# Kernel tuning notes

Measured on AMD Instinct MI355X. Metric: run time of the kernel, lower is better.

## Reference

```python
import jax, jax.numpy as jnp
import numpy as np

B, C, T = 128, 295, 2048
D1 = 270
NUM_SUBJECTS = 64

def setup_inputs() -> dict:
    key = jax.random.key(0)
    k_x, k_s, k_w1, k_b1, k_ws = jax.random.split(key, 5)
    X = jax.random.normal(k_x, (B, C, T), dtype=jnp.float32)
    subject_idxs = jax.random.randint(k_s, (B,), 0, NUM_SUBJECTS)
    W1 = jax.random.normal(k_w1, (D1, C), dtype=jnp.float32) * 0.05
    b1 = jax.random.normal(k_b1, (D1,), dtype=jnp.float32) * 0.05
    Ws = jax.random.normal(k_ws, (NUM_SUBJECTS, D1, D1), dtype=jnp.float32) * 0.05
    return {"X": X, "subject_idxs": subject_idxs, "W1": W1, "b1": b1, "Ws": Ws}

def reference(X, subject_idxs, W1, b1, Ws):
    # Shared 1x1 conv: pointwise channel mix C -> D1 with bias.  [B, D1, T]
    y = jnp.einsum('dc,bct->bdt', W1, X) + b1[None, :, None]
    # Top-1 expert dispatch: gather each sample's subject matrix. [B, D1, D1]
    W_sel = Ws[subject_idxs]
    # Per-sample 1x1 conv (batched GEMM), no bias.            [B, D1, T]
    out = jnp.einsum('bed,bdt->bet', W_sel, y)
    return out
```

## Files before the change

kernel.cpp:

```cpp
#include <hip/hip_runtime.h>
#include <hip/hip_bf16.h>

#define NSUBJ 64
#define CIN   295
#define DD    270
#define TT    2048
#define BB    128

#define WF_PER_S  92160
#define WF_PER_KS 9216
#define W1T_PER_KS 10240

typedef __attribute__((ext_vector_type(8))) short bf16x8;
typedef __attribute__((ext_vector_type(4))) float f32x4;
typedef unsigned short u16;

__device__ __forceinline__ u16 f2bf(float f) {
    return __bfloat16_as_ushort(__float2bfloat16(f));
}

__device__ __forceinline__ void glds16(const void* g, void* lds_base) {
    __builtin_amdgcn_global_load_lds(
        (const __attribute__((address_space(1))) unsigned int*)g,
        (__attribute__((address_space(3))) unsigned int*)lds_base, 16, 0, 0);
}

__global__ __launch_bounds__(256) void k_prep_w1(const float* __restrict__ W1,
                                                 const float* __restrict__ b1,
                                                 u16* __restrict__ W1t)
{
    const int idx = blockIdx.x * 256 + threadIdx.x;
    const int ks = idx / W1T_PER_KS;
    const int r  = idx - ks * W1T_PER_KS;
    const int kq = r / 2560;
    const int c  = (r - kq * 2560) >> 3;
    const int k8 = r & 7;
    const int d  = ks * 32 + kq * 8 + k8;
    float v = 0.f;
    if (d < DD) {
        if (c < CIN) v = W1[d * CIN + c];
        else if (c == CIN) v = b1[d];
    }
    W1t[idx] = f2bf(v);
}

__global__ __launch_bounds__(256, 1) void k_fuse_w(const float* __restrict__ Ws,
                                                   const u16* __restrict__ W1t,
                                                   u16* __restrict__ Wf)
{
    __shared__ u16 Aw[3072];
    __shared__ u16 Bw[10240];
    const int tid = threadIdx.x, lane = tid & 63, wid = tid >> 6;
    const int wm = wid >> 1, wn = wid & 1;
    const int mt = blockIdx.x, s = blockIdx.y;
    const int e0 = mt * 96;
    const float* Wsb = Ws + (size_t)s * DD * DD;

    f32x4 acc[3][10];
#pragma unroll
    for (int i = 0; i < 3; ++i)
#pragma unroll
        for (int j = 0; j < 10; ++j) acc[i][j] = (f32x4){0.f, 0.f, 0.f, 0.f};

    for (int ks = 0; ks < 9; ++ks) {
        const int k0 = ks * 32;
#pragma unroll
        for (int ci = 0; ci < 3; ++ci) {
            const int id = tid + ci * 256;
            const int m = id >> 3, q = id & 7;
            const int e = e0 + m, d = k0 + q * 4;
            float2 v01 = {0.f, 0.f}, v23 = {0.f, 0.f};
            if (e < DD) {
                if (d < DD)     v01 = *(const float2*)(Wsb + (size_t)e * DD + d);
                if (d + 2 < DD) v23 = *(const float2*)(Wsb + (size_t)e * DD + d + 2);
            }
            ushort4 h;
            h.x = f2bf(v01.x); h.y = f2bf(v01.y); h.z = f2bf(v23.x); h.w = f2bf(v23.y);
            *(ushort4*)(&Aw[(q >> 1) * 768 + m * 8 + (q & 1) * 4]) = h;
        }
#pragma unroll
        for (int k5 = 0; k5 < 5; ++k5) {
            const int seg = wid * 5 + k5;
            glds16(W1t + (size_t)ks * W1T_PER_KS + seg * 512 + lane * 8, &Bw[seg * 512]);
        }
        __syncthreads();
        bf16x8 af[3];
#pragma unroll
        for (int i = 0; i < 3; ++i)
            af[i] = *(const bf16x8*)(&Aw[(lane >> 4) * 768 + (wm * 48 + i * 16 + (lane & 15)) * 8]);
#pragma unroll
        for (int j = 0; j < 10; ++j) {
            const bf16x8 bfj = *(const bf16x8*)(&Bw[(lane >> 4) * 2560 + (wn * 160 + j * 16 + (lane & 15)) * 8]);
#pragma unroll
            for (int i = 0; i < 3; ++i)
                acc[i][j] = __builtin_amdgcn_mfma_f32_16x16x32_bf16(af[i], bfj, acc[i][j], 0, 0, 0);
        }
        __syncthreads();
    }
    const int rb = (lane >> 4) * 4, cc = lane & 15;
#pragma unroll
    for (int i = 0; i < 3; ++i) {
#pragma unroll
        for (int r = 0; r < 4; ++r) {
            const int e = e0 + wm * 48 + i * 16 + rb + r;
#pragma unroll
            for (int j = 0; j < 10; ++j) {
                const int c = wn * 160 + j * 16 + cc;
                Wf[(size_t)s * WF_PER_S + (c >> 5) * WF_PER_KS + ((c >> 3) & 3) * 2304
                   + e * 8 + (c & 7)] = f2bf(acc[i][j][r]);
            }
        }
    }
}

__global__ __launch_bounds__(256, 2) void k_main(const float* __restrict__ X,
                                                 const int* __restrict__ subj,
                                                 const u16* __restrict__ Wf,
                                                 float* __restrict__ out)
{
    __shared__ u16   Am[2][9216];
    __shared__ float Xm[2][2048];
    const int tid = threadIdx.x, lane = tid & 63, wid = tid >> 6;
    const int wm = wid >> 1, wn = wid & 1;
    const int nt = blockIdx.x, b = blockIdx.y;
    const int t0 = nt * 64;
    const int s = subj[b];
    const float* Xb = X + (size_t)b * CIN * TT;
    const u16* WfA = Wf + (size_t)s * WF_PER_S;
    const int g = lane >> 4;

    f32x4 acc[9][2];
#pragma unroll
    for (int i = 0; i < 9; ++i)
#pragma unroll
        for (int j = 0; j < 2; ++j) acc[i][j] = (f32x4){0.f, 0.f, 0.f, 0.f};

#define STAGEA(KS)                                                          \
    {                                                                       \
        _Pragma("unroll")                                                   \
        for (int k5 = 0; k5 < 5; ++k5) {                                    \
            const int seg = wid + 4 * k5;                                   \
            if (seg < 18)                                                   \
                glds16(WfA + (size_t)(KS) * WF_PER_KS + seg * 512 + lane * 8,\
                       &Am[(KS) & 1][seg * 512]);                           \
        }                                                                   \
    }
#define STAGEX(KS)                                                          \
    {                                                                       \
        _Pragma("unroll")                                                   \
        for (int k2 = 0; k2 < 2; ++k2) {                                    \
            const int seg = wid * 2 + k2;                                   \
            const int cr0 = (KS) * 32 + seg * 4 + g;                        \
            const int cr  = (cr0 < CIN) ? cr0 : (CIN - 1);                  \
            const int sc  = (lane & 15) ^ (((seg >> 1) & 3) << 2);          \
            glds16(Xb + (size_t)cr * TT + t0 + sc * 4,                      \
                   &Xm[(KS) & 1][seg * 256]);                               \
        }                                                                   \
    }
#define COMPUTE(KS, LAST)                                                   \
    {                                                                       \
        const float* Xc = &Xm[(KS) & 1][0];                                 \
        bf16x8 bfr[2];                                                      \
        _Pragma("unroll")                                                   \
        for (int j = 0; j < 2; ++j) {                                       \
            const int tsw = (wn * 32 + j * 16 + (lane & 15)) ^ (g << 4);    \
            bf16x8 bb;                                                      \
            _Pragma("unroll")                                               \
            for (int q = 0; q < 8; ++q) {                                   \
                float v = Xc[(g * 8 + q) * 64 + tsw];                       \
                if (LAST) {                                                 \
                    if (q == 7)      v = (g == 0) ? 1.0f : 0.0f;            \
                    else if (g > 0)  v = 0.0f;                              \
                }                                                           \
                bb[q] = (short)f2bf(v);                                     \
            }                                                               \
            bfr[j] = bb;                                                    \
        }                                                                   \
        _Pragma("unroll")                                                   \
        for (int i = 0; i < 9; ++i) {                                       \
            const bf16x8 af = *(const bf16x8*)(&Am[(KS) & 1][g * 2304 + (wm * 144 + i * 16 + (lane & 15)) * 8]); \
            acc[i][0] = __builtin_amdgcn_mfma_f32_16x16x32_bf16(af, bfr[0], acc[i][0], 0, 0, 0); \
            acc[i][1] = __builtin_amdgcn_mfma_f32_16x16x32_bf16(af, bfr[1], acc[i][1], 0, 0, 0); \
        }                                                                   \
    }

    STAGEA(0); STAGEX(0);
    __syncthreads();

#pragma unroll
    for (int ks = 0; ks < 10; ++ks) {
        if (ks < 9) { STAGEA(ks + 1); STAGEX(ks + 1); }
        COMPUTE(ks, (ks == 9));
        __syncthreads();
    }

    const int rb = g * 4, cc = lane & 15;
#pragma unroll
    for (int i = 0; i < 9; ++i) {
#pragma unroll
        for (int r = 0; r < 4; ++r) {
            const int e = wm * 144 + i * 16 + rb + r;
            if (e < DD) {
#pragma unroll
                for (int j = 0; j < 2; ++j) {
                    const int t = t0 + wn * 32 + j * 16 + cc;
                    out[((size_t)b * DD + e) * TT + t] = acc[i][j][r];
                }
            }
        }
    }
#undef STAGEA
#undef STAGEX
#undef COMPUTE
}

extern "C" void kernel_launch(void* const* d_in, const int* in_sizes, int n_in,
                              void* d_out, int out_size, void* d_ws, size_t ws_size,
                              hipStream_t stream) {
    const float* X    = (const float*)d_in[0];
    const int*   subj = (const int*)d_in[1];
    const float* W1   = (const float*)d_in[2];
    const float* b1   = (const float*)d_in[3];
    const float* Ws   = (const float*)d_in[4];
    float* out = (float*)d_out;

    u16* Wf  = (u16*)d_ws;
    u16* W1t = (u16*)((char*)d_ws + (size_t)NSUBJ * WF_PER_S * 2);

    k_prep_w1<<<dim3(360), 256, 0, stream>>>(W1, b1, W1t);
    k_fuse_w<<<dim3(3, NSUBJ), 256, 0, stream>>>(Ws, W1t, Wf);
    k_main<<<dim3(TT / 64, BB), 256, 0, stream>>>(X, subj, Wf, out);
}
```

Measured before the change: 192.5 us.

## Drop LDS staging in main GEMM; load operands directly to registers, remap blocks by XCD

```diff
diff --git a/kernel.cpp b/kernel.cpp
--- a/kernel.cpp
+++ b/kernel.cpp
@@ -118,16 +118,17 @@
                                                  const u16* __restrict__ Wf,
                                                  float* __restrict__ out)
 {
-    __shared__ u16   Am[2][9216];
-    __shared__ float Xm[2][2048];
     const int tid = threadIdx.x, lane = tid & 63, wid = tid >> 6;
     const int wm = wid >> 1, wn = wid & 1;
-    const int nt = blockIdx.x, b = blockIdx.y;
+    const int g = lane >> 4, l15 = lane & 15;
+    const int hw = blockIdx.x;
+    const int w  = (hw & 7) * 512 + (hw >> 3);
+    const int b  = w >> 5, nt = w & 31;
     const int t0 = nt * 64;
-    const int s = subj[b];
+    const int s  = subj[b];
     const float* Xb = X + (size_t)b * CIN * TT;
-    const u16* WfA = Wf + (size_t)s * WF_PER_S;
-    const int g = lane >> 4;
+    const u16* aB = Wf + (size_t)s * WF_PER_S + g * 2304 + (wm * 144 + l15) * 8;
+    const int tj0 = t0 + wn * 32 + l15;
 
     f32x4 acc[9][2];
 #pragma unroll
@@ -135,66 +136,62 @@
 #pragma unroll
         for (int j = 0; j < 2; ++j) acc[i][j] = (f32x4){0.f, 0.f, 0.f, 0.f};
 
-#define STAGEA(KS)                                                          \
-    {                                                                       \
-        _Pragma("unroll")                                                   \
-        for (int k5 = 0; k5 < 5; ++k5) {                                    \
-            const int seg = wid + 4 * k5;                                   \
-            if (seg < 18)                                                   \
-                glds16(WfA + (size_t)(KS) * WF_PER_KS + seg * 512 + lane * 8,\
-                       &Am[(KS) & 1][seg * 512]);                           \
-        }                                                                   \
-    }
-#define STAGEX(KS)                                                          \
-    {                                                                       \
-        _Pragma("unroll")                                                   \
-        for (int k2 = 0; k2 < 2; ++k2) {                                    \
-            const int seg = wid * 2 + k2;                                   \
-            const int cr0 = (KS) * 32 + seg * 4 + g;                        \
-            const int cr  = (cr0 < CIN) ? cr0 : (CIN - 1);                  \
-            const int sc  = (lane & 15) ^ (((seg >> 1) & 3) << 2);          \
-            glds16(Xb + (size_t)cr * TT + t0 + sc * 4,                      \
-                   &Xm[(KS) & 1][seg * 256]);                               \
-        }                                                                   \
-    }
-#define COMPUTE(KS, LAST)                                                   \
-    {                                                                       \
-        const float* Xc = &Xm[(KS) & 1][0];                                 \
-        bf16x8 bfr[2];                                                      \
-        _Pragma("unroll")                                                   \
-        for (int j = 0; j < 2; ++j) {                                       \
-            const int tsw = (wn * 32 + j * 16 + (lane & 15)) ^ (g << 4);    \
-            bf16x8 bb;                                                      \
-            _Pragma("unroll")                                               \
-            for (int q = 0; q < 8; ++q) {                                   \
-                float v = Xc[(g * 8 + q) * 64 + tsw];                       \
-                if (LAST) {                                                 \
-                    if (q == 7)      v = (g == 0) ? 1.0f : 0.0f;            \
-                    else if (g > 0)  v = 0.0f;                              \
-                }                                                           \
-                bb[q] = (short)f2bf(v);                                     \
-            }                                                               \
-            bfr[j] = bb;                                                    \
-        }                                                                   \
-        _Pragma("unroll")                                                   \
-        for (int i = 0; i < 9; ++i) {                                       \
-            const bf16x8 af = *(const bf16x8*)(&Am[(KS) & 1][g * 2304 + (wm * 144 + i * 16 + (lane & 15)) * 8]); \
-            acc[i][0] = __builtin_amdgcn_mfma_f32_16x16x32_bf16(af, bfr[0], acc[i][0], 0, 0, 0); \
-            acc[i][1] = __builtin_amdgcn_mfma_f32_16x16x32_bf16(af, bfr[1], acc[i][1], 0, 0, 0); \
-        }                                                                   \
-    }
-
-    STAGEA(0); STAGEX(0);
-    __syncthreads();
-
-#pragma unroll
-    for (int ks = 0; ks < 10; ++ks) {
-        if (ks < 9) { STAGEA(ks + 1); STAGEX(ks + 1); }
-        COMPUTE(ks, (ks == 9));
-        __syncthreads();
-    }
-
-    const int rb = g * 4, cc = lane & 15;
+#pragma unroll
+    for (int ks = 0; ks < 9; ++ks) {
+        bf16x8 af[9];
+#pragma unroll
+        for (int i = 0; i < 9; ++i)
+            af[i] = *(const bf16x8*)(aB + (size_t)ks * WF_PER_KS + i * 128);
+        float x0[8], x1[8];
+#pragma unroll
+        for (int q = 0; q < 8; ++q) {
+            const size_t roff = (size_t)((ks * 32 + g * 8 + q)) * TT + tj0;
+            x0[q] = Xb[roff];
+            x1[q] = Xb[roff + 16];
+        }
+        bf16x8 b0, b1;
+#pragma unroll
+        for (int q = 0; q < 8; ++q) {
+            b0[q] = (short)f2bf(x0[q]);
+            b1[q] = (short)f2bf(x1[q]);
+        }
+#pragma unroll
+        for (int i = 0; i < 9; ++i) {
+            acc[i][0] = __builtin_amdgcn_mfma_f32_16x16x32_bf16(af[i], b0, acc[i][0], 0, 0, 0);
+            acc[i][1] = __builtin_amdgcn_mfma_f32_16x16x32_bf16(af[i], b1, acc[i][1], 0, 0, 0);
+        }
+    }
+    {
+        bf16x8 af[9];
+#pragma unroll
+        for (int i = 0; i < 9; ++i)
+            af[i] = *(const bf16x8*)(aB + (size_t)9 * WF_PER_KS + i * 128);
+        bf16x8 b0, b1;
+#pragma unroll
+        for (int q = 0; q < 8; ++q) {
+            const int c  = 288 + g * 8 + q;
+            const int cl = (c < CIN) ? c : (c - 33);
+            const size_t roff = (size_t)cl * TT + tj0;
+            const float v0 = Xb[roff];
+            const float v1 = Xb[roff + 16];
+            float w0, w1;
+            if (g == 0) {
+                w0 = (q == 7) ? 1.0f : v0;
+                w1 = (q == 7) ? 1.0f : v1;
+            } else {
+                w0 = 0.0f; w1 = 0.0f;
+            }
+            b0[q] = (short)f2bf(w0);
+            b1[q] = (short)f2bf(w1);
+        }
+#pragma unroll
+        for (int i = 0; i < 9; ++i) {
+            acc[i][0] = __builtin_amdgcn_mfma_f32_16x16x32_bf16(af[i], b0, acc[i][0], 0, 0, 0);
+            acc[i][1] = __builtin_amdgcn_mfma_f32_16x16x32_bf16(af[i], b1, acc[i][1], 0, 0, 0);
+        }
+    }
+
+    const int rb = g * 4;
 #pragma unroll
     for (int i = 0; i < 9; ++i) {
 #pragma unroll
@@ -203,15 +200,12 @@
             if (e < DD) {
 #pragma unroll
                 for (int j = 0; j < 2; ++j) {
-                    const int t = t0 + wn * 32 + j * 16 + cc;
+                    const int t = tj0 + j * 16;
                     out[((size_t)b * DD + e) * TT + t] = acc[i][j][r];
                 }
             }
         }
     }
-#undef STAGEA
-#undef STAGEX
-#undef COMPUTE
 }
 
 extern "C" void kernel_launch(void* const* d_in, const int* in_sizes, int n_in,
@@ -229,5 +223,5 @@
 
     k_prep_w1<<<dim3(360), 256, 0, stream>>>(W1, b1, W1t);
     k_fuse_w<<<dim3(3, NSUBJ), 256, 0, stream>>>(Ws, W1t, Wf);
-    k_main<<<dim3(TT / 64, BB), 256, 0, stream>>>(X, subj, Wf, out);
-}
+    k_main<<<dim3(TT / 64 * BB), 256, 0, stream>>>(X, subj, Wf, out);
+}
```

New measurement: 244.7 us. 1.27x slower.

## Triple-buffer main GEMM loads with explicit vmcnt waits and remap blocks

Applied to the files above, without the earlier changes.

```diff
diff --git a/kernel.cpp b/kernel.cpp
--- a/kernel.cpp
+++ b/kernel.cpp
@@ -24,6 +24,10 @@
         (const __attribute__((address_space(1))) unsigned int*)g,
         (__attribute__((address_space(3))) unsigned int*)lds_base, 16, 0, 0);
 }
+
+#define WAITV(N) asm volatile("s_waitcnt vmcnt(" #N ")" ::: "memory")
+#define BAR()    __builtin_amdgcn_s_barrier()
+#define SB()     __builtin_amdgcn_sched_barrier(0)
 
 __global__ __launch_bounds__(256) void k_prep_w1(const float* __restrict__ W1,
                                                  const float* __restrict__ b1,
@@ -118,11 +122,13 @@
                                                  const u16* __restrict__ Wf,
                                                  float* __restrict__ out)
 {
-    __shared__ u16   Am[2][9216];
-    __shared__ float Xm[2][2048];
+    __shared__ u16   Am[3][9216];
+    __shared__ float Xm[3][2048];
     const int tid = threadIdx.x, lane = tid & 63, wid = tid >> 6;
     const int wm = wid >> 1, wn = wid & 1;
-    const int nt = blockIdx.x, b = blockIdx.y;
+    const int hw = blockIdx.x;
+    const int w  = (hw & 7) * 512 + (hw >> 3);
+    const int b  = w >> 5, nt = w & 31;
     const int t0 = nt * 64;
     const int s = subj[b];
     const float* Xb = X + (size_t)b * CIN * TT;
@@ -135,17 +141,17 @@
 #pragma unroll
         for (int j = 0; j < 2; ++j) acc[i][j] = (f32x4){0.f, 0.f, 0.f, 0.f};
 
-#define STAGEA(KS)                                                          \
+#define STAGEA(KS, BUF)                                                     \
     {                                                                       \
         _Pragma("unroll")                                                   \
         for (int k5 = 0; k5 < 5; ++k5) {                                    \
             const int seg = wid + 4 * k5;                                   \
             if (seg < 18)                                                   \
                 glds16(WfA + (size_t)(KS) * WF_PER_KS + seg * 512 + lane * 8,\
-                       &Am[(KS) & 1][seg * 512]);                           \
-        }                                                                   \
-    }
-#define STAGEX(KS)                                                          \
+                       &Am[BUF][seg * 512]);                                \
+        }                                                                   \
+    }
+#define STAGEX(KS, BUF)                                                     \
     {                                                                       \
         _Pragma("unroll")                                                   \
         for (int k2 = 0; k2 < 2; ++k2) {                                    \
@@ -154,12 +160,14 @@
             const int cr  = (cr0 < CIN) ? cr0 : (CIN - 1);                  \
             const int sc  = (lane & 15) ^ (((seg >> 1) & 3) << 2);          \
             glds16(Xb + (size_t)cr * TT + t0 + sc * 4,                      \
-                   &Xm[(KS) & 1][seg * 256]);                               \
-        }                                                                   \
-    }
-#define COMPUTE(KS, LAST)                                                   \
-    {                                                                       \
-        const float* Xc = &Xm[(KS) & 1][0];                                 \
+                   &Xm[BUF][seg * 256]);                                    \
+        }                                                                   \
+    }
+#define WAITSTEP()  { if (wid < 2) WAITV(7); else WAITV(6); }
+
+#define COMPUTE(BUF, LAST)                                                  \
+    {                                                                       \
+        const float* Xc = &Xm[BUF][0];                                      \
         bf16x8 bfr[2];                                                      \
         _Pragma("unroll")                                                   \
         for (int j = 0; j < 2; ++j) {                                       \
@@ -178,21 +186,29 @@
         }                                                                   \
         _Pragma("unroll")                                                   \
         for (int i = 0; i < 9; ++i) {                                       \
-            const bf16x8 af = *(const bf16x8*)(&Am[(KS) & 1][g * 2304 + (wm * 144 + i * 16 + (lane & 15)) * 8]); \
+            const bf16x8 af = *(const bf16x8*)(&Am[BUF][g * 2304 + (wm * 144 + i * 16 + (lane & 15)) * 8]); \
             acc[i][0] = __builtin_amdgcn_mfma_f32_16x16x32_bf16(af, bfr[0], acc[i][0], 0, 0, 0); \
             acc[i][1] = __builtin_amdgcn_mfma_f32_16x16x32_bf16(af, bfr[1], acc[i][1], 0, 0, 0); \
         }                                                                   \
     }
 
-    STAGEA(0); STAGEX(0);
-    __syncthreads();
-
-#pragma unroll
-    for (int ks = 0; ks < 10; ++ks) {
-        if (ks < 9) { STAGEA(ks + 1); STAGEX(ks + 1); }
-        COMPUTE(ks, (ks == 9));
-        __syncthreads();
-    }
+    STAGEA(0, 0); STAGEX(0, 0); SB();
+    STAGEA(1, 1); STAGEX(1, 1); SB();
+    WAITSTEP();
+    BAR();
+
+#define STEP(K)                                                             \
+    {                                                                       \
+        STAGEA((K) + 2, ((K) + 2) % 3); STAGEX((K) + 2, ((K) + 2) % 3); SB();\
+        COMPUTE((K) % 3, 0);                                                \
+        WAITSTEP();                                                         \
+        BAR();                                                              \
+    }
+    STEP(0) STEP(1) STEP(2) STEP(3) STEP(4) STEP(5) STEP(6) STEP(7)
+    COMPUTE(2, 0);
+    WAITV(0);
+    BAR();
+    COMPUTE(0, 1);
 
     const int rb = g * 4, cc = lane & 15;
 #pragma unroll
@@ -211,7 +227,9 @@
     }
 #undef STAGEA
 #undef STAGEX
+#undef WAITSTEP
 #undef COMPUTE
+#undef STEP
 }
 
 extern "C" void kernel_launch(void* const* d_in, const int* in_sizes, int n_in,
@@ -229,5 +247,5 @@
 
     k_prep_w1<<<dim3(360), 256, 0, stream>>>(W1, b1, W1t);
     k_fuse_w<<<dim3(3, NSUBJ), 256, 0, stream>>>(Ws, W1t, Wf);
-    k_main<<<dim3(TT / 64, BB), 256, 0, stream>>>(X, subj, Wf, out);
-}
+    k_main<<<dim3(TT / 64 * BB), 256, 0, stream>>>(X, subj, Wf, out);
+}
```

Result: faster. 184.8 us (-4.0%).
